# Kernel optimization log

Hardware: AMD Instinct MI355X
Metric: run time of the kernel (lower is better)

The kernel has to match this reference:

```python
import jax, jax.numpy as jnp
import numpy as np

N = 10000        # nodes
E = 320000       # edges (avg degree 32)
IN = 739         # in_channels
C = 64           # hid_channels
H = 1            # heads
D = C // H       # per-head dim
L = 10           # layer_num
G = 64           # num graphs in batch
LAMBD = 1.0


def setup_inputs() -> dict:
    key = jax.random.key(0)
    ks = jax.random.split(key, 14)
    s = 0.05
    return {
        "x": jax.random.normal(ks[0], (N, IN), jnp.float32),
        "edge_index": jax.random.randint(ks[1], (2, E), 0, N, dtype=jnp.int32),
        "batch": jnp.sort(jax.random.randint(ks[2], (N,), 0, G, dtype=jnp.int32)),
        # InitFeat: Linear(739->64), ELU, Linear(64->64) (dropout = identity at eval)
        "w0": jax.random.normal(ks[3], (IN, C), jnp.float32) * s,
        "b0": jax.random.normal(ks[4], (C,), jnp.float32) * s,
        "w1": jax.random.normal(ks[5], (C, C), jnp.float32) * s,
        "b1": jax.random.normal(ks[6], (C,), jnp.float32) * s,
        # AeroConv attention vectors for k = 1..L-1
        "conv_att": jax.random.normal(ks[7], (L - 1, H, D), jnp.float32) * s,
        # UpdateZ k=0 (g = h, width D) and k=1..L-1 (g = [h, z_scale], width 2D)
        "hop_att0": jax.random.normal(ks[8], (H, D), jnp.float32) * s,
        "hop_bias0": jax.random.normal(ks[9], (H,), jnp.float32) * s,
        "hop_att": jax.random.normal(ks[10], (L - 1, H, 2 * D), jnp.float32) * s,
        "hop_bias": jax.random.normal(ks[11], (L - 1, H), jnp.float32) * s,
        # readout head Linear(64->1)
        "w_head": jax.random.normal(ks[12], (C, 1), jnp.float32) * s,
        "b_head": jax.random.normal(ks[13], (1,), jnp.float32) * s,
    }


def reference(x, edge_index, batch, w0, b0, w1, b1, conv_att,
              hop_att0, hop_bias0, hop_att, hop_bias, w_head, b_head):
    src, dst = edge_index[0], edge_index[1]

    # ---- InitFeat (dropout is identity at inference) ----
    h = x @ w0 + b0
    h = jax.nn.elu(h) @ w1 + b1              # [N, C]
    x = h

    # ---- UpdateZ, k = 0: z = h * hop_attention ----
    hh = x.reshape(N, H, D)
    attn = jnp.sum(hop_att0 * jax.nn.elu(hh), axis=-1) + hop_bias0   # [N, H]
    z = hh * attn[..., None]                 # [N, H, D]

    for i in range(L - 1):
        k = i + 1
        scale = jnp.float32(np.log(LAMBD / k + 1.0 + 1e-6))
        z_scale = z * scale                  # [N, H, D]

        # per-edge attention: elu(z_i + z_j), dot with att, softplus
        a = jax.nn.elu(z_scale[src] + z_scale[dst])                   # [E, H, D]
        a = jax.nn.softplus(jnp.sum(conv_att[i] * a, axis=-1)) + 1e-6  # [E, H]

        # symmetric normalization by scatter-summed degree
        adj_sum = jax.ops.segment_sum(a, dst, num_segments=N)         # [N, H]
        inv = jnp.maximum(adj_sum, 1e-32) ** -0.5
        na = (inv[src] * a * inv[dst])[..., None]                     # [E, H, 1]

        # weighted scatter-sum of source features
        msgs = x[src].reshape(E, H, D) * na                           # [E, H, D]
        x = jax.ops.segment_sum(msgs, dst, num_segments=N).reshape(N, C)

        # UpdateZ (k >= 1): g = [h, z_scale]
        hh = x.reshape(N, H, D)
        g = jnp.concatenate([hh, z_scale], axis=-1)                   # [N, H, 2D]
        attn = jnp.sum(hop_att[i] * jax.nn.elu(g), axis=-1) + hop_bias[i]
        z = z + hh * attn[..., None]

    # ---- readout: elu, global mean pool over batch, linear head ----
    zf = jax.nn.elu(z.reshape(N, C))
    seg_sum = jax.ops.segment_sum(zf, batch, num_segments=G)          # [G, C]
    cnt = jax.ops.segment_sum(jnp.ones((N,), zf.dtype), batch, num_segments=G)
    pooled = seg_sum / jnp.maximum(cnt, 1.0)[:, None]
    return pooled @ w_head + b_head                                   # [G, 1]
```

## Files before the change

### kernel.cpp

```cpp
#include <hip/hip_runtime.h>
#include <hip/hip_bf16.h>
#include <math.h>

#define NN     10000
#define EE     320000
#define IN_CH  739
#define CC     64
#define GG     64
#define NLAYER 9

__device__ __forceinline__ float eluf(float x) {
    return x > 0.f ? x : __expf(x) - 1.f;
}
__device__ __forceinline__ float softplusf(float x) {
    return fmaxf(x, 0.f) + __logf(1.f + __expf(-fabsf(x)));
}
__device__ __forceinline__ float wave_sum(float v) {
#pragma unroll
    for (int off = 32; off > 0; off >>= 1) v += __shfl_xor(v, off, 64);
    return v;
}

__global__ __launch_bounds__(256) void k_gemm1_part(
    const float* __restrict__ x, const float* __restrict__ w0,
    float* __restrict__ hpart)
{
    __shared__ float xs[64 * 68];
    __shared__ float ws[64 * 64];
    const int tid = threadIdx.x;
    const int cg = tid & 15;
    const int rg = tid >> 4;
    const int split = blockIdx.x & 3;
    const int R0 = (blockIdx.x >> 2) * 64;
    const int K0 = split * 192;

    const int sk = tid & 63;
    const int sr = tid >> 6;

    float xr[16], wr[16];
    float acc[4][4] = {};

#pragma unroll
    for (int i = 0; i < 16; ++i) {
        const int r = sr + 4 * i;
        const int gr = R0 + r;
        const int gk = K0 + sk;
        xr[i] = (gr < NN && gk < IN_CH) ? x[(size_t)gr * IN_CH + gk] : 0.f;
        const int wk = K0 + r;
        wr[i] = (wk < IN_CH) ? w0[wk * CC + sk] : 0.f;
    }

    for (int t = 0; t < 3; ++t) {
        __syncthreads();
#pragma unroll
        for (int i = 0; i < 16; ++i) {
            const int r = sr + 4 * i;
            xs[r * 68 + sk] = xr[i];
            ws[r * 64 + sk] = wr[i];
        }
        __syncthreads();
        if (t + 1 < 3) {
            const int k0 = K0 + (t + 1) * 64;
#pragma unroll
            for (int i = 0; i < 16; ++i) {
                const int r = sr + 4 * i;
                const int gr = R0 + r;
                const int gk = k0 + sk;
                xr[i] = (gr < NN && gk < IN_CH) ? x[(size_t)gr * IN_CH + gk] : 0.f;
                const int wk = k0 + r;
                wr[i] = (wk < IN_CH) ? w0[wk * CC + sk] : 0.f;
            }
        }
#pragma unroll 4
        for (int k4 = 0; k4 < 64; k4 += 4) {
            float4 xv[4], wv[4];
#pragma unroll
            for (int j = 0; j < 4; ++j)
                xv[j] = *(const float4*)&xs[(rg * 4 + j) * 68 + k4];
#pragma unroll
            for (int q = 0; q < 4; ++q)
                wv[q] = *(const float4*)&ws[(k4 + q) * 64 + cg * 4];
#pragma unroll
            for (int j = 0; j < 4; ++j) {
                const float* xf = (const float*)&xv[j];
#pragma unroll
                for (int q = 0; q < 4; ++q) {
                    const float* wf = (const float*)&wv[q];
#pragma unroll
                    for (int i = 0; i < 4; ++i)
                        acc[j][i] = fmaf(xf[q], wf[i], acc[j][i]);
                }
            }
        }
    }

#pragma unroll
    for (int j = 0; j < 4; ++j) {
        const int row = R0 + rg * 4 + j;
        if (row < NN)
            *(float4*)&hpart[((size_t)split * NN + row) * CC + cg * 4] =
                make_float4(acc[j][0], acc[j][1], acc[j][2], acc[j][3]);
    }
}

__global__ __launch_bounds__(256) void k_init2(
    const float* __restrict__ hpart,
    const float* __restrict__ b0, const float* __restrict__ w1,
    const float* __restrict__ b1,
    const float* __restrict__ hop_att0, const float* __restrict__ hop_bias0,
    float scale1,
    float* __restrict__ xout, float* __restrict__ zout,
    float* __restrict__ zsout)
{
    __shared__ float xs[32 * 68];
    __shared__ float ws[64 * 64];
    const int tid = threadIdx.x;
    const int R0 = blockIdx.x * 32;

#pragma unroll
    for (int j = 0; j < 2; ++j) {
        const int slot = tid + 256 * j;
        const int row = slot >> 4;
        const int col4 = (slot & 15) * 4;
        const int grow = R0 + row;
        float4 s = make_float4(0.f, 0.f, 0.f, 0.f);
        if (grow < NN) {
#pragma unroll
            for (int sp = 0; sp < 4; ++sp) {
                const float4 v =
                    *(const float4*)&hpart[((size_t)sp * NN + grow) * CC + col4];
                s.x += v.x; s.y += v.y; s.z += v.z; s.w += v.w;
            }
        }
        const float4 bb = *(const float4*)&b0[col4];
        s.x = eluf(s.x + bb.x); s.y = eluf(s.y + bb.y);
        s.z = eluf(s.z + bb.z); s.w = eluf(s.w + bb.w);
        *(float4*)&xs[row * 68 + col4] = s;
    }
    {
        const int sk = tid & 63;
        const int sr = tid >> 6;
#pragma unroll
        for (int i = 0; i < 16; ++i)
            ws[(sr + 4 * i) * 64 + sk] = w1[(sr + 4 * i) * CC + sk];
    }
    __syncthreads();

    const int cg = tid & 15;
    const int rg = tid >> 4;
    float acc2[2][4];
    const float4 b1v = *(const float4*)&b1[cg * 4];
#pragma unroll
    for (int j = 0; j < 2; ++j) {
        acc2[j][0] = b1v.x; acc2[j][1] = b1v.y;
        acc2[j][2] = b1v.z; acc2[j][3] = b1v.w;
    }
#pragma unroll 4
    for (int k4 = 0; k4 < 64; k4 += 4) {
        float4 xv[2], wv[4];
#pragma unroll
        for (int j = 0; j < 2; ++j)
            xv[j] = *(const float4*)&xs[(rg * 2 + j) * 68 + k4];
#pragma unroll
        for (int q = 0; q < 4; ++q)
            wv[q] = *(const float4*)&ws[(k4 + q) * 64 + cg * 4];
#pragma unroll
        for (int j = 0; j < 2; ++j) {
            const float* xf = (const float*)&xv[j];
#pragma unroll
            for (int q = 0; q < 4; ++q) {
                const float* wf = (const float*)&wv[q];
#pragma unroll
                for (int i = 0; i < 4; ++i)
                    acc2[j][i] = fmaf(xf[q], wf[i], acc2[j][i]);
            }
        }
    }

    __syncthreads();
#pragma unroll
    for (int j = 0; j < 2; ++j)
        *(float4*)&ws[(rg * 2 + j) * 64 + cg * 4] =
            make_float4(acc2[j][0], acc2[j][1], acc2[j][2], acc2[j][3]);
    __syncthreads();

    const int c = tid & 63;
    const int w = tid >> 6;
    const float ha = hop_att0[c];
    const float hb = hop_bias0[0];
#pragma unroll
    for (int rr = 0; rr < 8; ++rr) {
        const int r = w * 8 + rr;
        const float v = ws[r * 64 + c];
        const float attn = wave_sum(ha * eluf(v)) + hb;
        const int row = R0 + r;
        if (row < NN) {
            const float zv = v * attn;
            xout[row * CC + c] = v;
            zout[row * CC + c] = zv;
            zsout[row * CC + c] = zv * scale1;
        }
    }
}

__global__ __launch_bounds__(256) void k_hist(const int* __restrict__ ei,
                                              int* __restrict__ deg)
{
    const int e = blockIdx.x * 256 + threadIdx.x;
    atomicAdd(&deg[ei[EE + e]], 1);
}

__global__ __launch_bounds__(256) void k_scan(const int* __restrict__ deg,
                                              int* __restrict__ offs)
{
    __shared__ int part[256];
    const int tid = threadIdx.x;
    const int start = tid * 40;
    const int end = start + 40 < NN ? start + 40 : NN;
    int sum = 0;
    for (int i = start; i < end; ++i) sum += deg[i];
    part[tid] = sum;
    __syncthreads();
    if (tid == 0) {
        int run = 0;
        for (int i = 0; i < 256; ++i) { int t = part[i]; part[i] = run; run += t; }
    }
    __syncthreads();
    int run = part[tid];
    for (int i = start; i < end; ++i) { offs[i] = run; run += deg[i]; }
}

__global__ __launch_bounds__(256) void k_scatter(
    const int* __restrict__ ei, const int* __restrict__ offs,
    int* __restrict__ cursor, int* __restrict__ csr_src)
{
    const int e = blockIdx.x * 256 + threadIdx.x;
    const int d = ei[EE + e];
    const int pos = offs[d] + atomicAdd(&cursor[d], 1);
    csr_src[pos] = ei[e];
}

__global__ __launch_bounds__(256) void k_bounds(const int* __restrict__ batch,
                                                int* __restrict__ gstart)
{
    const int n = blockIdx.x * 256 + threadIdx.x;
    if (n >= NN) return;
    if (n == 0)
        for (int g = 0; g <= batch[0]; ++g) gstart[g] = 0;
    else {
        const int b0 = batch[n - 1], b1 = batch[n];
        for (int g = b0 + 1; g <= b1; ++g) gstart[g] = n;
    }
    if (n == NN - 1)
        for (int g = batch[NN - 1] + 1; g <= GG; ++g) gstart[g] = NN;
}

__global__ __launch_bounds__(256) void k_edge_adj(
    const int* __restrict__ offs, const int* __restrict__ deg,
    const int* __restrict__ csr_src,
    const float* __restrict__ zs_buf, const float* __restrict__ conv_att,
    float* __restrict__ a_csr, float* __restrict__ inv_adj)
{
    const int n = blockIdx.x * 4 + (threadIdx.x >> 6);
    const int lane = threadIdx.x & 63;
    const int l = lane & 15;
    const int grp = lane >> 4;
    const int start = offs[n];
    const int len = deg[n];

    const float4 zd = *(const float4*)(zs_buf + n * CC + l * 4);
    const float4 scv = *(const float4*)(conv_att + l * 4);

    float asum = 0.f;
    int i = grp;
    for (; i + 4 < len; i += 8) {
        const int s0 = csr_src[start + i];
        const int s1 = csr_src[start + i + 4];
        const float4 a0 = *(const float4*)(zs_buf + s0 * CC + l * 4);
        const float4 a1 = *(const float4*)(zs_buf + s1 * CC + l * 4);
        float p0 = scv.x * eluf(a0.x + zd.x);
        p0 = fmaf(scv.y, eluf(a0.y + zd.y), p0);
        p0 = fmaf(scv.z, eluf(a0.z + zd.z), p0);
        p0 = fmaf(scv.w, eluf(a0.w + zd.w), p0);
        float p1 = scv.x * eluf(a1.x + zd.x);
        p1 = fmaf(scv.y, eluf(a1.y + zd.y), p1);
        p1 = fmaf(scv.z, eluf(a1.z + zd.z), p1);
        p1 = fmaf(scv.w, eluf(a1.w + zd.w), p1);
#pragma unroll
        for (int off = 8; off > 0; off >>= 1) {
            p0 += __shfl_xor(p0, off, 64);
            p1 += __shfl_xor(p1, off, 64);
        }
        const float ae0 = softplusf(p0) + 1e-6f;
        const float ae1 = softplusf(p1) + 1e-6f;
        asum += ae0 + ae1;
        if (l == 0) {
            a_csr[start + i] = ae0;
            a_csr[start + i + 4] = ae1;
        }
    }
    for (; i < len; i += 4) {
        const int s0 = csr_src[start + i];
        const float4 a0 = *(const float4*)(zs_buf + s0 * CC + l * 4);
        float p0 = scv.x * eluf(a0.x + zd.x);
        p0 = fmaf(scv.y, eluf(a0.y + zd.y), p0);
        p0 = fmaf(scv.z, eluf(a0.z + zd.z), p0);
        p0 = fmaf(scv.w, eluf(a0.w + zd.w), p0);
#pragma unroll
        for (int off = 8; off > 0; off >>= 1) p0 += __shfl_xor(p0, off, 64);
        const float ae0 = softplusf(p0) + 1e-6f;
        asum += ae0;
        if (l == 0) a_csr[start + i] = ae0;
    }

    asum += __shfl_xor(asum, 16, 64);
    asum += __shfl_xor(asum, 32, 64);
    if (lane == 0) inv_adj[n] = rsqrtf(fmaxf(asum, 1e-32f));
}

__global__ __launch_bounds__(256) void k_msg_fused(
    const int* __restrict__ offs, const int* __restrict__ deg,
    const int* __restrict__ csr_src, const float* __restrict__ a_csr,
    const float* __restrict__ inv_adj, const float* __restrict__ x,
    float* __restrict__ xn, float* __restrict__ z,
    float* __restrict__ zs_buf,
    const float* __restrict__ hop_att, const float* __restrict__ hop_bias,
    float scale_next)
{
    const int n = blockIdx.x * 4 + (threadIdx.x >> 6);
    const int c = threadIdx.x & 63;
    const int start = offs[n];
    const int len = deg[n];
    const float invd = inv_adj[n];

    float acc = 0.f;
    for (int base = 0; base < len; base += 64) {
        const int cnt = (len - base) < 64 ? (len - base) : 64;
        int s_l = 0; float na_l = 0.f;
        if (c < cnt) {
            s_l = csr_src[start + base + c];
            na_l = a_csr[start + base + c] * inv_adj[s_l] * invd;
        }
        int j = 0;
        for (; j + 4 <= cnt; j += 4) {
            const int s0 = __builtin_amdgcn_readlane(s_l, j);
            const int s1 = __builtin_amdgcn_readlane(s_l, j + 1);
            const int s2 = __builtin_amdgcn_readlane(s_l, j + 2);
            const int s3 = __builtin_amdgcn_readlane(s_l, j + 3);
            const float n0 = __int_as_float(__builtin_amdgcn_readlane(__float_as_int(na_l), j));
            const float n1 = __int_as_float(__builtin_amdgcn_readlane(__float_as_int(na_l), j + 1));
            const float n2 = __int_as_float(__builtin_amdgcn_readlane(__float_as_int(na_l), j + 2));
            const float n3 = __int_as_float(__builtin_amdgcn_readlane(__float_as_int(na_l), j + 3));
            const float v0 = x[s0 * CC + c];
            const float v1 = x[s1 * CC + c];
            const float v2 = x[s2 * CC + c];
            const float v3 = x[s3 * CC + c];
            acc = fmaf(v0, n0, acc);
            acc = fmaf(v1, n1, acc);
            acc = fmaf(v2, n2, acc);
            acc = fmaf(v3, n3, acc);
        }
        for (; j < cnt; ++j) {
            const int s = __builtin_amdgcn_readlane(s_l, j);
            const float na = __int_as_float(__builtin_amdgcn_readlane(__float_as_int(na_l), j));
            acc = fmaf(x[s * CC + c], na, acc);
        }
    }

    const float zv = z[n * CC + c];
    const float zsv = zs_buf[n * CC + c];
    float g = hop_att[c] * eluf(acc) + hop_att[CC + c] * eluf(zsv);
    const float attn = wave_sum(g) + hop_bias[0];
    const float znew = zv + acc * attn;
    z[n * CC + c] = znew;
    zs_buf[n * CC + c] = znew * scale_next;
    xn[n * CC + c] = acc;
}

__global__ __launch_bounds__(256) void k_pool_head(
    const float* __restrict__ z, const int* __restrict__ gstart,
    const float* __restrict__ w_head, const float* __restrict__ b_head,
    float* __restrict__ out)
{
    __shared__ float red[4][CC];
    const int g = blockIdx.x;
    const int w = threadIdx.x >> 6;
    const int c = threadIdx.x & 63;
    const int s0 = gstart[g], s1 = gstart[g + 1];

    float acc = 0.f;
    for (int n = s0 + w; n < s1; n += 4) acc += eluf(z[n * CC + c]);
    red[w][c] = acc;
    __syncthreads();
    if (w == 0) {
        const float v = red[0][c] + red[1][c] + red[2][c] + red[3][c];
        const float tot = wave_sum(v * w_head[c]);
        if (c == 0)
            out[g] = tot / fmaxf((float)(s1 - s0), 1.f) + b_head[0];
    }
}

extern "C" void kernel_launch(void* const* d_in, const int* in_sizes, int n_in,
                              void* d_out, int out_size, void* d_ws, size_t ws_size,
                              hipStream_t stream) {
    const float* x        = (const float*)d_in[0];
    const int*   ei       = (const int*)d_in[1];
    const int*   batch    = (const int*)d_in[2];
    const float* w0       = (const float*)d_in[3];
    const float* b0       = (const float*)d_in[4];
    const float* w1       = (const float*)d_in[5];
    const float* b1       = (const float*)d_in[6];
    const float* conv_att = (const float*)d_in[7];
    const float* hop_att0 = (const float*)d_in[8];
    const float* hop_bias0= (const float*)d_in[9];
    const float* hop_att  = (const float*)d_in[10];
    const float* hop_bias = (const float*)d_in[11];
    const float* w_head   = (const float*)d_in[12];
    const float* b_head   = (const float*)d_in[13];
    float* out = (float*)d_out;

    float sc[NLAYER + 1];
    for (int k = 1; k <= NLAYER; ++k)
        sc[k] = (float)log(1.0 / (double)k + 1.0 + 1e-6);

    float* xA      = (float*)d_ws;
    float* xB      = xA + NN * CC;
    float* zbuf    = xB + NN * CC;
    float* zsbuf   = zbuf + NN * CC;
    float* inv_adj = zsbuf + NN * CC;
    float* hpart   = inv_adj + NN;
    float* a_csr   = hpart;
    int*   csr_src = (int*)(a_csr + EE);
    int*   deg     = csr_src + EE;
    int*   cursor  = deg + NN;
    int*   offs    = cursor + NN;
    int*   gstart  = offs + NN;

    k_gemm1_part<<<157 * 4, 256, 0, stream>>>(x, w0, hpart);
    k_init2<<<313, 256, 0, stream>>>(hpart, b0, w1, b1, hop_att0, hop_bias0,
                                     sc[1], xA, zbuf, zsbuf);

    hipMemsetAsync(deg, 0, (size_t)(2 * NN) * 4, stream);
    k_hist<<<EE / 256, 256, 0, stream>>>(ei, deg);
    k_scan<<<1, 256, 0, stream>>>(deg, offs);
    k_scatter<<<EE / 256, 256, 0, stream>>>(ei, offs, cursor, csr_src);
    k_bounds<<<(NN + 255) / 256, 256, 0, stream>>>(batch, gstart);

    float* xcur = xA;
    float* xnext = xB;
    for (int i = 0; i < NLAYER; ++i) {
        const float scale_next = (i + 1 < NLAYER) ? sc[i + 2] : 0.f;
        k_edge_adj<<<NN / 4, 256, 0, stream>>>(offs, deg, csr_src, zsbuf,
                                               conv_att + i * CC,
                                               a_csr, inv_adj);
        k_msg_fused<<<NN / 4, 256, 0, stream>>>(offs, deg, csr_src, a_csr,
                                                inv_adj, xcur, xnext, zbuf,
                                                zsbuf,
                                                hop_att + i * 2 * CC,
                                                hop_bias + i, scale_next);
        float* t = xcur; xcur = xnext; xnext = t;
    }

    k_pool_head<<<GG, 256, 0, stream>>>(zbuf, gstart, w_head, b_head, out);
}
```

Measured before the change: 473.6 us.

## Build CSR via two-level bucketed partition and deepen gather unrolling

Replaces the per-edge global-atomic CSR scatter with a two-pass partition. Each block first groups edges by 64-node destination bucket in shared memory and writes them in coalesced runs. A second pass then places source ids per destination using shared-memory atomics, which is meant to reduce global atomic contention and scattered writes. It also raises the unroll depth in the edge-attention loop (4 edges per group) and in the message gather loop (8 loads in flight) to improve memory-level parallelism. The cost is an extra int2 staging buffer, one more kernel launch, and higher register pressure.

Result: faster. 445.1 us (-6.0%).

```diff
diff --git a/kernel.cpp b/kernel.cpp
--- a/kernel.cpp
+++ b/kernel.cpp
@@ -8,6 +8,8 @@
 #define CC     64
 #define GG     64
 #define NLAYER 9
+#define NBUCK  157
+#define CHUNK  2048
 
 __device__ __forceinline__ float eluf(float x) {
     return x > 0.f ? x : __expf(x) - 1.f;
@@ -211,7 +213,8 @@
 }
 
 __global__ __launch_bounds__(256) void k_scan(const int* __restrict__ deg,
-                                              int* __restrict__ offs)
+                                              int* __restrict__ offs,
+                                              int* __restrict__ bcur)
 {
     __shared__ int part[256];
     const int tid = threadIdx.x;
@@ -227,17 +230,87 @@
     }
     __syncthreads();
     int run = part[tid];
-    for (int i = start; i < end; ++i) { offs[i] = run; run += deg[i]; }
-}
-
-__global__ __launch_bounds__(256) void k_scatter(
-    const int* __restrict__ ei, const int* __restrict__ offs,
-    int* __restrict__ cursor, int* __restrict__ csr_src)
-{
-    const int e = blockIdx.x * 256 + threadIdx.x;
-    const int d = ei[EE + e];
-    const int pos = offs[d] + atomicAdd(&cursor[d], 1);
-    csr_src[pos] = ei[e];
+    for (int i = start; i < end; ++i) {
+        offs[i] = run;
+        if ((i & 63) == 0) bcur[i >> 6] = run;
+        run += deg[i];
+    }
+}
+
+__global__ __launch_bounds__(256) void k_part1(
+    const int* __restrict__ ei, int* __restrict__ bcur,
+    int2* __restrict__ csr_pair)
+{
+    __shared__ int hist[NBUCK];
+    __shared__ int scan_s[NBUCK];
+    __shared__ int base_g[NBUCK];
+    __shared__ int lcur[NBUCK];
+    __shared__ int2 staged[CHUNK];
+    const int tid = threadIdx.x;
+    const int e0 = blockIdx.x * CHUNK;
+
+    for (int b = tid; b < NBUCK; b += 256) { hist[b] = 0; lcur[b] = 0; }
+    __syncthreads();
+
+    int src[8], dst[8];
+#pragma unroll
+    for (int j = 0; j < 8; ++j) {
+        const int e = e0 + tid + 256 * j;
+        if (e < EE) {
+            src[j] = ei[e];
+            dst[j] = ei[EE + e];
+            atomicAdd(&hist[dst[j] >> 6], 1);
+        } else dst[j] = -1;
+    }
+    __syncthreads();
+    if (tid == 0) {
+        int run = 0;
+        for (int b = 0; b < NBUCK; ++b) { scan_s[b] = run; run += hist[b]; }
+    }
+    __syncthreads();
+    if (tid < NBUCK && hist[tid] > 0)
+        base_g[tid] = atomicAdd(&bcur[tid], hist[tid]);
+    __syncthreads();
+#pragma unroll
+    for (int j = 0; j < 8; ++j) {
+        if (dst[j] >= 0) {
+            const int b = dst[j] >> 6;
+            const int r = atomicAdd(&lcur[b], 1);
+            staged[scan_s[b] + r] = make_int2(src[j], dst[j]);
+        }
+    }
+    __syncthreads();
+    const int tot = (EE - e0) < CHUNK ? (EE - e0) : CHUNK;
+    for (int i = tid; i < tot; i += 256) {
+        const int2 p = staged[i];
+        const int b = p.y >> 6;
+        csr_pair[base_g[b] + (i - scan_s[b])] = p;
+    }
+}
+
+__global__ __launch_bounds__(256) void k_part2(
+    const int* __restrict__ offs, const int2* __restrict__ csr_pair,
+    int* __restrict__ csr_src)
+{
+    __shared__ int lcnt[64];
+    __shared__ int loffs[64];
+    const int b = blockIdx.x;
+    const int tid = threadIdx.x;
+    const int d0 = b * 64;
+    if (tid < 64) {
+        lcnt[tid] = 0;
+        const int d = d0 + tid;
+        loffs[tid] = (d < NN) ? offs[d] : EE;
+    }
+    __syncthreads();
+    const int r0 = offs[d0];
+    const int r1 = (d0 + 64 < NN) ? offs[d0 + 64] : EE;
+    for (int i = r0 + tid; i < r1; i += 256) {
+        const int2 p = csr_pair[i];
+        const int ld = p.y & 63;
+        const int r = atomicAdd(&lcnt[ld], 1);
+        csr_src[loffs[ld] + r] = p.x;
+    }
 }
 
 __global__ __launch_bounds__(256) void k_bounds(const int* __restrict__ batch,
@@ -273,11 +346,15 @@
 
     float asum = 0.f;
     int i = grp;
-    for (; i + 4 < len; i += 8) {
+    for (; i + 12 < len; i += 16) {
         const int s0 = csr_src[start + i];
         const int s1 = csr_src[start + i + 4];
+        const int s2 = csr_src[start + i + 8];
+        const int s3 = csr_src[start + i + 12];
         const float4 a0 = *(const float4*)(zs_buf + s0 * CC + l * 4);
         const float4 a1 = *(const float4*)(zs_buf + s1 * CC + l * 4);
+        const float4 a2 = *(const float4*)(zs_buf + s2 * CC + l * 4);
+        const float4 a3 = *(const float4*)(zs_buf + s3 * CC + l * 4);
         float p0 = scv.x * eluf(a0.x + zd.x);
         p0 = fmaf(scv.y, eluf(a0.y + zd.y), p0);
         p0 = fmaf(scv.z, eluf(a0.z + zd.z), p0);
@@ -286,17 +363,31 @@
         p1 = fmaf(scv.y, eluf(a1.y + zd.y), p1);
         p1 = fmaf(scv.z, eluf(a1.z + zd.z), p1);
         p1 = fmaf(scv.w, eluf(a1.w + zd.w), p1);
+        float p2 = scv.x * eluf(a2.x + zd.x);
+        p2 = fmaf(scv.y, eluf(a2.y + zd.y), p2);
+        p2 = fmaf(scv.z, eluf(a2.z + zd.z), p2);
+        p2 = fmaf(scv.w, eluf(a2.w + zd.w), p2);
+        float p3 = scv.x * eluf(a3.x + zd.x);
+        p3 = fmaf(scv.y, eluf(a3.y + zd.y), p3);
+        p3 = fmaf(scv.z, eluf(a3.z + zd.z), p3);
+        p3 = fmaf(scv.w, eluf(a3.w + zd.w), p3);
 #pragma unroll
         for (int off = 8; off > 0; off >>= 1) {
             p0 += __shfl_xor(p0, off, 64);
             p1 += __shfl_xor(p1, off, 64);
+            p2 += __shfl_xor(p2, off, 64);
+            p3 += __shfl_xor(p3, off, 64);
         }
         const float ae0 = softplusf(p0) + 1e-6f;
         const float ae1 = softplusf(p1) + 1e-6f;
-        asum += ae0 + ae1;
+        const float ae2 = softplusf(p2) + 1e-6f;
+        const float ae3 = softplusf(p3) + 1e-6f;
+        asum += ae0 + ae1 + ae2 + ae3;
         if (l == 0) {
             a_csr[start + i] = ae0;
             a_csr[start + i + 4] = ae1;
+            a_csr[start + i + 8] = ae2;
+            a_csr[start + i + 12] = ae3;
         }
     }
     for (; i < len; i += 4) {
@@ -342,27 +433,24 @@
             na_l = a_csr[start + base + c] * inv_adj[s_l] * invd;
         }
         int j = 0;
-        for (; j + 4 <= cnt; j += 4) {
-            const int s0 = __builtin_amdgcn_readlane(s_l, j);
-            const int s1 = __builtin_amdgcn_readlane(s_l, j + 1);
-            const int s2 = __builtin_amdgcn_readlane(s_l, j + 2);
-            const int s3 = __builtin_amdgcn_readlane(s_l, j + 3);
-            const float n0 = __int_as_float(__builtin_amdgcn_readlane(__float_as_int(na_l), j));
-            const float n1 = __int_as_float(__builtin_amdgcn_readlane(__float_as_int(na_l), j + 1));
-            const float n2 = __int_as_float(__builtin_amdgcn_readlane(__float_as_int(na_l), j + 2));
-            const float n3 = __int_as_float(__builtin_amdgcn_readlane(__float_as_int(na_l), j + 3));
-            const float v0 = x[s0 * CC + c];
-            const float v1 = x[s1 * CC + c];
-            const float v2 = x[s2 * CC + c];
-            const float v3 = x[s3 * CC + c];
-            acc = fmaf(v0, n0, acc);
-            acc = fmaf(v1, n1, acc);
-            acc = fmaf(v2, n2, acc);
-            acc = fmaf(v3, n3, acc);
+        for (; j + 8 <= cnt; j += 8) {
+            int ss[8]; float nn_[8];
+#pragma unroll
+            for (int q = 0; q < 8; ++q) {
+                ss[q] = __builtin_amdgcn_readlane(s_l, j + q);
+                nn_[q] = __int_as_float(
+                    __builtin_amdgcn_readlane(__float_as_int(na_l), j + q));
+            }
+            float vv[8];
+#pragma unroll
+            for (int q = 0; q < 8; ++q) vv[q] = x[ss[q] * CC + c];
+#pragma unroll
+            for (int q = 0; q < 8; ++q) acc = fmaf(vv[q], nn_[q], acc);
         }
         for (; j < cnt; ++j) {
             const int s = __builtin_amdgcn_readlane(s_l, j);
-            const float na = __int_as_float(__builtin_amdgcn_readlane(__float_as_int(na_l), j));
+            const float na = __int_as_float(
+                __builtin_amdgcn_readlane(__float_as_int(na_l), j));
             acc = fmaf(x[s * CC + c], na, acc);
         }
     }
@@ -431,19 +519,21 @@
     float* hpart   = inv_adj + NN;
     float* a_csr   = hpart;
     int*   csr_src = (int*)(a_csr + EE);
-    int*   deg     = csr_src + EE;
-    int*   cursor  = deg + NN;
-    int*   offs    = cursor + NN;
-    int*   gstart  = offs + NN;
+    int2*  csr_pair= (int2*)(csr_src + EE);
+    int*   deg     = (int*)(csr_pair + EE);
+    int*   offs    = deg + NN;
+    int*   bcur    = offs + NN;
+    int*   gstart  = bcur + NBUCK;
 
     k_gemm1_part<<<157 * 4, 256, 0, stream>>>(x, w0, hpart);
     k_init2<<<313, 256, 0, stream>>>(hpart, b0, w1, b1, hop_att0, hop_bias0,
                                      sc[1], xA, zbuf, zsbuf);
 
-    hipMemsetAsync(deg, 0, (size_t)(2 * NN) * 4, stream);
+    hipMemsetAsync(deg, 0, (size_t)NN * 4, stream);
     k_hist<<<EE / 256, 256, 0, stream>>>(ei, deg);
-    k_scan<<<1, 256, 0, stream>>>(deg, offs);
-    k_scatter<<<EE / 256, 256, 0, stream>>>(ei, offs, cursor, csr_src);
+    k_scan<<<1, 256, 0, stream>>>(deg, offs, bcur);
+    k_part1<<<(EE + CHUNK - 1) / CHUNK, 256, 0, stream>>>(ei, bcur, csr_pair);
+    k_part2<<<NBUCK, 256, 0, stream>>>(offs, csr_pair, csr_src);
     k_bounds<<<(NN + 255) / 256, 256, 0, stream>>>(batch, gstart);
 
     float* xcur = xA;
```
